# Performance work log

Measured on AMD Instinct MI355X. Metric: run time of the kernel, lower is better.

Reference implementation:

```python
import jax, jax.numpy as jnp
import numpy as np

D = 1024           # fusion_dim
H_MHA = 16         # fusion_heads
H_GAT = 8          # graph attention heads
GAT_DH = D // H_GAT
DIL = (1, 2, 4, 8, 16)
K = 7              # temporal_kernel_size
B, T = 8, 256


def setup_inputs() -> dict:
    key = jax.random.key(0)
    ks = jax.random.split(key, 20)

    def w(k, sh, fan):
        return jax.random.normal(k, sh, jnp.float32) * np.float32(1.0 / np.sqrt(fan))

    inp = {"features": jax.random.normal(ks[0], (B, T, D), jnp.float32)}
    for i, dil in enumerate(DIL):
        inp["conv_w%d" % i] = w(ks[1 + i], (D, D, K), D * K)   # torch Conv1d (out, in, k)
        inp["conv_b%d" % i] = jnp.zeros((D,), jnp.float32)
    inp["fp_w"] = w(ks[6], (D, 5 * D), 5 * D)                    # torch Linear (out, in)
    inp["fp_b"] = jnp.zeros((D,), jnp.float32)
    inp["ln_g"] = jnp.ones((D,), jnp.float32)
    inp["ln_b"] = jnp.zeros((D,), jnp.float32)
    inp["wq"] = w(ks[7], (D, D), D); inp["bq"] = jnp.zeros((D,), jnp.float32)
    inp["wk"] = w(ks[8], (D, D), D); inp["bk"] = jnp.zeros((D,), jnp.float32)
    inp["wv"] = w(ks[9], (D, D), D); inp["bv"] = jnp.zeros((D,), jnp.float32)
    inp["wo"] = w(ks[10], (D, D), D); inp["bo"] = jnp.zeros((D,), jnp.float32)
    inp["gat_w"] = w(ks[11], (D, D), D)
    inp["gat_b"] = jnp.zeros((D,), jnp.float32)
    # original `a` is (2*head_dim, 1) shared across heads; split into a1 (source) / a2 (target)
    inp["gat_a1"] = w(ks[12], (GAT_DH,), 2 * GAT_DH)
    inp["gat_a2"] = w(ks[13], (GAT_DH,), 2 * GAT_DH)
    return inp


def _forward(features, conv_ws, conv_bs, fp_w, fp_b, ln_g, ln_b,
             wq, bq, wk, bk, wv, bv, wo, bo, gat_w, gat_b, gat_a1, gat_a2):
    Bb, Tt, Dm = features.shape
    x = jnp.transpose(features, (0, 2, 1))                       # (B, D, T)
    feats = []
    for wgt, bias, dil in zip(conv_ws, conv_bs, DIL):
        pad = (K - 1) * dil // 2                                 # 'same' padding
        y = jax.lax.conv_general_dilated(
            x, wgt, window_strides=(1,), padding=[(pad, pad)],
            rhs_dilation=(dil,), dimension_numbers=("NCH", "OIH", "NCH"))
        feats.append(jnp.transpose(y + bias[None, :, None], (0, 2, 1)))
    ms = jnp.concatenate(feats, axis=-1)                         # (B, T, 5D)
    z = ms @ fp_w.T + fp_b                                       # (B, T, D)
    mu = jnp.mean(z, -1, keepdims=True)
    var = jnp.var(z, -1, keepdims=True)
    z = (z - mu) * jax.lax.rsqrt(var + 1e-5) * ln_g + ln_b       # LayerNorm
    z = jax.nn.gelu(z, approximate=False)
    # --- multi-head self attention (batch_first, no dropout at eval) ---
    dh = Dm // H_MHA
    q = (z @ wq.T + bq).reshape(Bb, Tt, H_MHA, dh)
    k = (z @ wk.T + bk).reshape(Bb, Tt, H_MHA, dh)
    v = (z @ wv.T + bv).reshape(Bb, Tt, H_MHA, dh)
    scores = jnp.einsum("bqhd,bkhd->bhqk", q, k) * np.float32(1.0 / np.sqrt(dh))
    attn = jax.nn.softmax(scores, axis=-1)
    ctx = jnp.einsum("bhqk,bkhd->bqhd", attn, v).reshape(Bb, Tt, Dm)
    att_out = ctx @ wo.T + bo
    # --- all-pairs graph attention over N = B*T nodes (GAT-style, a shared across heads) ---
    n = Bb * Tt
    hg = (att_out.reshape(n, Dm) @ gat_w.T + gat_b).reshape(n, H_GAT, GAT_DH)
    e1 = jnp.einsum("nhd,d->nh", hg, gat_a1)                     # a1 . h_i
    e2 = jnp.einsum("nhd,d->nh", hg, gat_a2)                     # a2 . h_j
    e = jax.nn.leaky_relu(e1[:, None, :] + e2[None, :, :], 0.2)  # (N, N, H) via broadcast
    alpha = jax.nn.softmax(e, axis=1)                            # normalize over j
    hp = jnp.einsum("ijh,jhd->ihd", alpha, hg).reshape(n, Dm)
    g = jax.nn.elu(hp).reshape(Bb, Tt, Dm)
    return g + features


def reference(features, conv_w0, conv_w1, conv_w2, conv_w3, conv_w4,
              conv_b0, conv_b1, conv_b2, conv_b3, conv_b4,
              fp_w, fp_b, ln_g, ln_b,
              wq, bq, wk, bk, wv, bv, wo, bo,
              gat_w, gat_b, gat_a1, gat_a2):
    return _forward(features,
                    (conv_w0, conv_w1, conv_w2, conv_w3, conv_w4),
                    (conv_b0, conv_b1, conv_b2, conv_b3, conv_b4),
                    fp_w, fp_b, ln_g, ln_b,
                    wq, bq, wk, bk, wv, bv, wo, bo,
                    gat_w, gat_b, gat_a1, gat_a2)
```

## Files before the change

kernel.cpp:

```cpp
#include <hip/hip_runtime.h>
#include <hip/hip_bf16.h>

typedef __bf16 bf16_t;
typedef bf16_t bf16x8 __attribute__((ext_vector_type(8)));
typedef bf16_t bf16x4v __attribute__((ext_vector_type(4)));
typedef float f32x4 __attribute__((ext_vector_type(4)));

__device__ __forceinline__ void gll16(const bf16_t* g, bf16_t* l) {
    __builtin_amdgcn_global_load_lds(
        (const __attribute__((address_space(1))) unsigned int*)g,
        (__attribute__((address_space(3))) unsigned int*)l, 16, 0, 0);
}

__global__ __launch_bounds__(256)
void cvt_f32_bf16(const float* __restrict__ in, bf16_t* __restrict__ out, int n4)
{
    int i = blockIdx.x * 256 + threadIdx.x;
    if (i < n4) {
        float4 v = ((const float4*)in)[i];
        bf16x4v o = { (bf16_t)v.x, (bf16_t)v.y, (bf16_t)v.z, (bf16_t)v.w };
        *(bf16x4v*)&out[i * 4] = o;
    }
}

__global__ __launch_bounds__(256)
void cvt_multi(const float* __restrict__ fpw, const float* __restrict__ wq,
               const float* __restrict__ wk, const float* __restrict__ wv,
               const float* __restrict__ wo, const float* __restrict__ gw,
               bf16_t* __restrict__ fpwb, bf16_t* __restrict__ wqb,
               bf16_t* __restrict__ wkb, bf16_t* __restrict__ wvb,
               bf16_t* __restrict__ wob, bf16_t* __restrict__ gwb)
{
    int id = blockIdx.x * 256 + threadIdx.x;
    const float* src; bf16_t* dst; int off;
    if (id < 1310720) { src = fpw; dst = fpwb; off = id; }
    else {
        int id3 = id - 1310720;
        int w = id3 >> 18; off = id3 & 262143;
        const float* ss[5] = {wq, wk, wv, wo, gw};
        bf16_t* dd[5] = {wqb, wkb, wvb, wob, gwb};
        src = ss[w]; dst = dd[w];
    }
    float4 v = ((const float4*)src)[off];
    bf16x4v o = { (bf16_t)v.x, (bf16_t)v.y, (bf16_t)v.z, (bf16_t)v.w };
    *(bf16x4v*)&dst[off * 4] = o;
}

__global__ __launch_bounds__(256)
void reorder_convw(const float* w0, const float* w1, const float* w2,
                   const float* w3, const float* w4, bf16_t* __restrict__ out)
{
    int gid = blockIdx.x * 256 + threadIdx.x;
    int i = gid / 1835008;
    int w = gid - i * 1835008;
    int o = w / 1792;
    int r2 = w - o * 1792;
    int kk = r2 >> 8, c4 = (r2 & 255) * 4;
    const float* ws[5] = {w0, w1, w2, w3, w4};
    const float* src = ws[i] + (size_t)o * 7168 + c4 * 7 + kk;
    bf16x4v v = { (bf16_t)src[0], (bf16_t)src[7], (bf16_t)src[14], (bf16_t)src[21] };
    *(bf16x4v*)&out[((size_t)(i * 7 + kk) << 20) + (o << 10) + c4] = v;
}

__global__ __launch_bounds__(256)
void gather_bias(const float* b0, const float* b1, const float* b2,
                 const float* b3, const float* b4,
                 const float* bq, const float* bk,
                 float* __restrict__ out, float* __restrict__ qkbias,
                 bf16_t* __restrict__ zp)
{
    int idx = blockIdx.x * 256 + threadIdx.x;
    if (blockIdx.x == 0 && threadIdx.x < 32) zp[threadIdx.x] = (bf16_t)0.0f;
    if (idx < 5120) {
        const float* bs[5] = {b0, b1, b2, b3, b4};
        out[idx] = bs[idx >> 10][idx & 1023];
    } else {
        int j = idx - 5120;
        qkbias[j] = (j < 1024) ? bq[j] : bk[j - 1024];
    }
}

template<bool CONV, bool OUT_BF16, bool BIAS_ROW = false, int NR = 128>
__global__ __launch_bounds__(256)
void mfma_gemm(const bf16_t* __restrict__ A, const bf16_t* __restrict__ Bw,
               const float* __restrict__ bias, void* __restrict__ outv,
               const bf16_t* __restrict__ zp,
               int Kd, int lda, int ldb, int ldo, int out_col0)
{
    constexpr int FN = NR / 32;
    __shared__ __align__(16) bf16_t As[3][NR * 32];
    __shared__ __align__(16) bf16_t Bs[3][128 * 32];
    const int t = threadIdx.x;
    const int lane = t & 63, wave = t >> 6;
    const int wn = (wave & 1) * (NR / 2), wm = (wave >> 1) * 64;
    const int q = lane >> 4, lr = lane & 15;
    const int mt = CONV ? (blockIdx.x & 7) : blockIdx.x;
    const int conv_i = CONV ? (blockIdx.x >> 3) : 0;
    const int m0 = mt * 128, n0 = blockIdx.y * NR;
    const int srow = lane >> 2, sseg = lane & 3;
    const int sw_seg = sseg ^ ((srow >> 1) & 3);
    const int slotq = (q ^ ((lr >> 1) & 3)) * 8;

    f32x4 acc[FN][4];
    #pragma unroll
    for (int a = 0; a < FN; a++)
        #pragma unroll
        for (int b = 0; b < 4; b++) acc[a][b] = (f32x4){0.f, 0.f, 0.f, 0.f};

    const int ksteps = Kd >> 5;
    const int T = CONV ? ksteps * 7 : ksteps;

    int s_tap = 0, s_k0 = 0;
    auto do_stage = [&](int bi) {
        const bf16_t* Bp = CONV ? (Bw + ((size_t)(conv_i * 7 + s_tap) << 20)) : Bw;
        const int shift = CONV ? ((s_tap - 3) << conv_i) : 0;
        #pragma unroll
        for (int p = 0; p < NR / 64; p++) {
            const int slab = p * 64 + wave * 16;
            const bf16_t* ga;
            if (CONV) {
                const int slabN = n0 + slab;
                const int inSeg = slabN & 255;
                if (inSeg + shift >= 0 && inSeg + shift <= 240) {
                    ga = A + (size_t)(slabN + srow + shift) * lda + s_k0 + sw_seg * 8;
                } else {
                    int n = slabN + srow;
                    int tg = (n & 255) + shift;
                    ga = ((unsigned)tg < 256u)
                       ? A + (size_t)((n & ~255) + tg) * lda + s_k0 + sw_seg * 8
                       : zp + sseg * 8;
                }
            } else {
                ga = A + (size_t)(n0 + slab + srow) * lda + s_k0 + sw_seg * 8;
            }
            gll16(ga, &As[bi][slab * 32]);
        }
        #pragma unroll
        for (int p = 0; p < 2; p++) {
            const int slab = p * 64 + wave * 16;
            const int rr = slab + srow;
            gll16(Bp + (size_t)(m0 + rr) * ldb + s_k0 + sw_seg * 8, &Bs[bi][slab * 32]);
        }
        s_k0 += 32;
        if (CONV && s_k0 == Kd) { s_k0 = 0; s_tap++; }
    };

    do_stage(0);
    do_stage(1);

    int cur = 0;
    for (int s = 0; s < T; s++) {
        if (s + 1 < T) {
            if constexpr (NR == 128) asm volatile("s_waitcnt vmcnt(4)" ::: "memory");
            else                     asm volatile("s_waitcnt vmcnt(3)" ::: "memory");
        } else {
            asm volatile("s_waitcnt vmcnt(0)" ::: "memory");
        }
        __builtin_amdgcn_s_barrier();
        __builtin_amdgcn_sched_barrier(0);

        bf16x8 af[FN], bfv[4];
        #pragma unroll
        for (int f = 0; f < FN; f++)
            af[f] = *(bf16x8*)&As[cur][(wn + f * 16 + lr) * 32 + slotq];
        #pragma unroll
        for (int f = 0; f < 4; f++)
            bfv[f] = *(bf16x8*)&Bs[cur][(wm + f * 16 + lr) * 32 + slotq];

        int nb = cur + 2; if (nb >= 3) nb -= 3;
        if (s + 2 < T) do_stage(nb);

        __builtin_amdgcn_s_setprio(1);
        #pragma unroll
        for (int fn = 0; fn < FN; fn++)
            #pragma unroll
            for (int fm = 0; fm < 4; fm++)
                acc[fn][fm] = __builtin_amdgcn_mfma_f32_16x16x32_bf16(
                    af[fn], bfv[fm], acc[fn][fm], 0, 0, 0);
        __builtin_amdgcn_s_setprio(0);
        cur++; if (cur == 3) cur = 0;
    }

    const int oc0 = CONV ? (conv_i << 10) : out_col0;
    #pragma unroll
    for (int fn = 0; fn < FN; fn++) {
        #pragma unroll
        for (int r = 0; r < 4; r++) {
            int n = n0 + wn + fn * 16 + q * 4 + r;
            #pragma unroll
            for (int fm = 0; fm < 4; fm++) {
                int m = m0 + wm + fm * 16 + lr;
                float v = acc[fn][fm][r];
                if (bias) v += bias[BIAS_ROW ? n : (oc0 + m)];
                if (OUT_BF16)
                    ((bf16_t*)outv)[(size_t)n * ldo + oc0 + m] = (bf16_t)v;
                else
                    ((float*)outv)[(size_t)n * ldo + oc0 + m] = v;
            }
        }
    }
}

__global__ __launch_bounds__(256)
void ln_gelu(float* __restrict__ z, bf16_t* __restrict__ zb,
             const float* __restrict__ g, const float* __restrict__ b)
{
    __shared__ float r1[256], r2[256];
    const int n = blockIdx.x, t = threadIdx.x;
    float* row = z + (size_t)n * 1024;
    float x[4], s = 0.f, s2 = 0.f;
    #pragma unroll
    for (int u = 0; u < 4; u++) {
        x[u] = row[t + u * 256];
        s += x[u]; s2 += x[u] * x[u];
    }
    r1[t] = s; r2[t] = s2;
    __syncthreads();
    for (int off = 128; off > 0; off >>= 1) {
        if (t < off) { r1[t] += r1[t + off]; r2[t] += r2[t + off]; }
        __syncthreads();
    }
    const float mu  = r1[0] * (1.0f / 1024.0f);
    const float var = r2[0] * (1.0f / 1024.0f) - mu * mu;
    const float rstd = rsqrtf(var + 1e-5f);
    #pragma unroll
    for (int u = 0; u < 4; u++) {
        int c = t + u * 256;
        float y = (x[u] - mu) * rstd * g[c] + b[c];
        float gv = 0.5f * y * (1.0f + erff(y * 0.70710678118654752f));
        row[c] = gv;
        zb[(size_t)n * 1024 + c] = (bf16_t)gv;
    }
}

__global__ __launch_bounds__(256)
void attn_mfma(const bf16_t* __restrict__ qg, const bf16_t* __restrict__ kg,
               const bf16_t* __restrict__ vt, bf16_t* __restrict__ ctx)
{
    const int it = blockIdx.x, h = blockIdx.y, bb = blockIdx.z;
    const int t = threadIdx.x, lane = t & 63, wave = t >> 6;
    const int q4 = lane >> 4, lr = lane & 15;
    const size_t qkbase = (size_t)bb * 256 * 2048 + (size_t)h * 64;

    __shared__ __align__(16) bf16_t Qs[4][32 * 64];
    __shared__ __align__(16) bf16_t Ks[64 * 64];
    __shared__ __align__(16) bf16_t Vs[64 * 64];
    __shared__ __align__(16) bf16_t Ps[4][32 * 64];

    {
        const int itbase = it * 128;
        #pragma unroll
        for (int rep = 0; rep < 4; rep++) {
            int idx = rep * 256 + t;
            int rl = idx >> 3, seg = idx & 7;
            bf16x8 v = *(const bf16x8*)&qg[qkbase + (size_t)(itbase + rl) * 2048 + seg * 8];
            *(bf16x8*)&Qs[rl >> 5][(rl & 31) * 64 + ((seg ^ (rl & 7)) << 3)] = v;
        }
    }

    f32x4 o[2][4];
    float mrow[2][4], lrow[2][4];
    #pragma unroll
    for (int fn = 0; fn < 2; fn++)
        #pragma unroll
        for (int x = 0; x < 4; x++) {
            o[fn][x] = (f32x4){0.f, 0.f, 0.f, 0.f};
            mrow[fn][x] = -1e30f; lrow[fn][x] = 0.f;
        }

    for (int j0 = 0; j0 < 256; j0 += 64) {
        __syncthreads();
        #pragma unroll
        for (int rep = 0; rep < 2; rep++) {
            int idx = rep * 256 + t;
            int rl = idx >> 3, seg = idx & 7;
            bf16x8 kv = *(const bf16x8*)&kg[qkbase + (size_t)(j0 + rl) * 2048 + seg * 8];
            *(bf16x8*)&Ks[rl * 64 + ((seg ^ (rl & 7)) << 3)] = kv;
            bf16x8 vv = *(const bf16x8*)&vt[(size_t)(h * 64 + rl) * 2048 + bb * 256 + j0 + seg * 8];
            *(bf16x8*)&Vs[rl * 64 + ((seg ^ (rl & 7)) << 3)] = vv;
        }
        __syncthreads();

        f32x4 s[2][4];
        #pragma unroll
        for (int fn = 0; fn < 2; fn++)
            #pragma unroll
            for (int fm = 0; fm < 4; fm++) s[fn][fm] = (f32x4){0.f, 0.f, 0.f, 0.f};
        #pragma unroll
        for (int kk = 0; kk < 2; kk++) {
            bf16x8 aq[2], bk[4];
            #pragma unroll
            for (int fn = 0; fn < 2; fn++) {
                int row = fn * 16 + lr;
                aq[fn] = *(bf16x8*)&Qs[wave][row * 64 + (((kk * 4 + q4) ^ (row & 7)) << 3)];
            }
            #pragma unroll
            for (int fm = 0; fm < 4; fm++) {
                int row = fm * 16 + lr;
                bk[fm] = *(bf16x8*)&Ks[row * 64 + (((kk * 4 + q4) ^ (row & 7)) << 3)];
            }
            #pragma unroll
            for (int fn = 0; fn < 2; fn++)
                #pragma unroll
                for (int fm = 0; fm < 4; fm++)
                    s[fn][fm] = __builtin_amdgcn_mfma_f32_16x16x32_bf16(
                        aq[fn], bk[fm], s[fn][fm], 0, 0, 0);
        }

        #pragma unroll
        for (int fn = 0; fn < 2; fn++) {
            #pragma unroll
            for (int r = 0; r < 4; r++) {
                float sv[4];
                #pragma unroll
                for (int fm = 0; fm < 4; fm++) sv[fm] = s[fn][fm][r] * 0.125f;
                float rm = fmaxf(fmaxf(sv[0], sv[1]), fmaxf(sv[2], sv[3]));
                rm = fmaxf(rm, __shfl_xor(rm, 1));
                rm = fmaxf(rm, __shfl_xor(rm, 2));
                rm = fmaxf(rm, __shfl_xor(rm, 4));
                rm = fmaxf(rm, __shfl_xor(rm, 8));
                float mold = mrow[fn][r];
                float mnew = fmaxf(mold, rm);
                float scl = __expf(mold - mnew);
                mrow[fn][r] = mnew;
                int prow = fn * 16 + q4 * 4 + r;
                float psum = 0.f;
                #pragma unroll
                for (int fm = 0; fm < 4; fm++) {
                    float p = __expf(sv[fm] - mnew);
                    psum += p;
                    int col = fm * 16 + lr;
                    Ps[wave][prow * 64 + (col ^ ((prow & 7) << 3))] = (bf16_t)p;
                }
                psum += __shfl_xor(psum, 1);
                psum += __shfl_xor(psum, 2);
                psum += __shfl_xor(psum, 4);
                psum += __shfl_xor(psum, 8);
                lrow[fn][r] = lrow[fn][r] * scl + psum;
                #pragma unroll
                for (int fd = 0; fd < 4; fd++) o[fn][fd][r] *= scl;
            }
        }

        #pragma unroll
        for (int kk = 0; kk < 2; kk++) {
            bf16x8 ap[2], bvf[4];
            #pragma unroll
            for (int fn = 0; fn < 2; fn++) {
                int row = fn * 16 + lr;
                ap[fn] = *(bf16x8*)&Ps[wave][row * 64 + (((kk * 4 + q4) ^ (row & 7)) << 3)];
            }
            #pragma unroll
            for (int fd = 0; fd < 4; fd++) {
                int row = fd * 16 + lr;
                bvf[fd] = *(bf16x8*)&Vs[row * 64 + (((kk * 4 + q4) ^ (row & 7)) << 3)];
            }
            #pragma unroll
            for (int fn = 0; fn < 2; fn++)
                #pragma unroll
                for (int fd = 0; fd < 4; fd++)
                    o[fn][fd] = __builtin_amdgcn_mfma_f32_16x16x32_bf16(
                        ap[fn], bvf[fd], o[fn][fd], 0, 0, 0);
        }
    }

    const int i0 = it * 128 + wave * 32;
    #pragma unroll
    for (int fn = 0; fn < 2; fn++) {
        #pragma unroll
        for (int r = 0; r < 4; r++) {
            float inv = 1.0f / lrow[fn][r];
            int row = i0 + fn * 16 + q4 * 4 + r;
            #pragma unroll
            for (int fd = 0; fd < 4; fd++) {
                int col = h * 64 + fd * 16 + lr;
                ctx[(size_t)bb * 262144 + (size_t)row * 1024 + col] =
                    (bf16_t)(o[fn][fd][r] * inv);
            }
        }
    }
}

__global__ __launch_bounds__(256)
void gat_e(const float* __restrict__ hg, const float* __restrict__ a1,
           const float* __restrict__ a2, float* __restrict__ e1t,
           float* __restrict__ e2t)
{
    int id = blockIdx.x * 256 + threadIdx.x;
    int h = id >> 11, n = id & 2047;
    const float* hr = hg + (size_t)n * 1024 + h * 128;
    float s1 = 0.f, s2 = 0.f;
    for (int d = 0; d < 128; d += 4) {
        float4 x = *(const float4*)&hr[d];
        float4 u1 = *(const float4*)&a1[d];
        float4 u2 = *(const float4*)&a2[d];
        s1 += x.x * u1.x + x.y * u1.y + x.z * u1.z + x.w * u1.w;
        s2 += x.x * u2.x + x.y * u2.y + x.z * u2.z + x.w * u2.w;
    }
    e1t[id] = s1; e2t[id] = s2;
}

__global__ __launch_bounds__(256)
void transpose_hg(const float* __restrict__ in, bf16_t* __restrict__ out)
{
    __shared__ float tile[32][33];
    const int t = threadIdx.x;
    const int j0 = blockIdx.x * 32, c0 = blockIdx.y * 32;
    {
        int jl = t >> 3, cl = (t & 7) * 4;
        float4 v = *(const float4*)(in + (size_t)(j0 + jl) * 1024 + c0 + cl);
        tile[jl][cl] = v.x; tile[jl][cl + 1] = v.y;
        tile[jl][cl + 2] = v.z; tile[jl][cl + 3] = v.w;
    }
    __syncthreads();
    {
        int cl = t >> 3, jl = (t & 7) * 4;
        bf16x4v o = { (bf16_t)tile[jl][cl], (bf16_t)tile[jl + 1][cl],
                      (bf16_t)tile[jl + 2][cl], (bf16_t)tile[jl + 3][cl] };
        *(bf16x4v*)&out[(size_t)(c0 + cl) * 2048 + j0 + jl] = o;
    }
}

__global__ __launch_bounds__(256)
void gat_agg_mfma(const bf16_t* __restrict__ hgT, const float* __restrict__ e1t,
                  const float* __restrict__ e2t, const float* __restrict__ feat,
                  float* __restrict__ outp)
{
    const int it = blockIdx.x, h = blockIdx.y;
    const int i0 = it * 64;
    __shared__ float e2s[2048];
    __shared__ float e1s[64], mS[64], lSinv[64];
    __shared__ float wmax[4];
    __shared__ __align__(16) bf16_t Ps[64 * 136];
    __shared__ __align__(16) bf16_t Hs[128 * 136];
    const int t = threadIdx.x;
    const int lane = t & 63, wave = t >> 6;
    const int q = lane >> 4, lr = lane & 15;
    const int wm = wave * 32;

    float lmax = -1e30f;
    for (int idx = t; idx < 2048; idx += 256) {
        float v = e2t[h * 2048 + idx];
        e2s[idx] = v;
        lmax = fmaxf(lmax, v);
    }
    if (t < 64) e1s[t] = e1t[h * 2048 + i0 + t];
    #pragma unroll
    for (int d = 1; d < 64; d <<= 1) lmax = fmaxf(lmax, __shfl_xor(lmax, d));
    if (lane == 0) wmax[wave] = lmax;
    __syncthreads();
    {
        float maxE2 = fmaxf(fmaxf(wmax[0], wmax[1]), fmaxf(wmax[2], wmax[3]));
        if (t < 64) {
            float x = e1s[t] + maxE2;
            mS[t] = (x >= 0.f) ? x : 0.2f * x;
        }
    }
    __syncthreads();

    f32x4 acc[4][2];
    #pragma unroll
    for (int a = 0; a < 4; a++)
        #pragma unroll
        for (int b = 0; b < 2; b++) acc[a][b] = (f32x4){0.f, 0.f, 0.f, 0.f};
    float psum[4] = {0.f, 0.f, 0.f, 0.f};

    for (int j0 = 0; j0 < 2048; j0 += 128) {
        for (int idx = t; idx < 2048; idx += 256) {
            int d = idx >> 4, seg = idx & 15;
            *(bf16x8*)&Hs[d * 136 + seg * 8] =
                *(const bf16x8*)&hgT[(size_t)(h * 128 + d) * 2048 + j0 + seg * 8];
        }
        #pragma unroll
        for (int rep = 0; rep < 4; rep++) {
            int idx = rep * 256 + t;
            int i = idx >> 4, jg = idx & 15;
            float ei = e1s[i], mi = mS[i];
            bf16x8 pv;
            #pragma unroll
            for (int u = 0; u < 8; u++) {
                float x = ei + e2s[j0 + jg * 8 + u];
                x = (x >= 0.f) ? x : 0.2f * x;
                float p = __expf(x - mi);
                psum[rep] += p;
                pv[u] = (bf16_t)p;
            }
            *(bf16x8*)&Ps[i * 136 + jg * 8] = pv;
        }
        __syncthreads();
        #pragma unroll
        for (int kb = 0; kb < 4; kb++) {
            bf16x8 af[4], bf2[2];
            #pragma unroll
            for (int fn = 0; fn < 4; fn++)
                af[fn] = *(bf16x8*)&Ps[(fn * 16 + lr) * 136 + kb * 32 + q * 8];
            #pragma unroll
            for (int fm = 0; fm < 2; fm++)
                bf2[fm] = *(bf16x8*)&Hs[(wm + fm * 16 + lr) * 136 + kb * 32 + q * 8];
            #pragma unroll
            for (int fn = 0; fn < 4; fn++)
                #pragma unroll
                for (int fm = 0; fm < 2; fm++)
                    acc[fn][fm] = __builtin_amdgcn_mfma_f32_16x16x32_bf16(
                        af[fn], bf2[fm], acc[fn][fm], 0, 0, 0);
        }
        __syncthreads();
    }

    #pragma unroll
    for (int rep = 0; rep < 4; rep++) {
        float v = psum[rep];
        v += __shfl_xor(v, 1);
        v += __shfl_xor(v, 2);
        v += __shfl_xor(v, 4);
        v += __shfl_xor(v, 8);
        if ((t & 15) == 0) lSinv[rep * 16 + (t >> 4)] = 1.0f / v;
    }
    __syncthreads();

    #pragma unroll
    for (int fn = 0; fn < 4; fn++) {
        #pragma unroll
        for (int r = 0; r < 4; r++) {
            int il = fn * 16 + q * 4 + r;
            int i = i0 + il;
            float inv = lSinv[il];
            #pragma unroll
            for (int fm = 0; fm < 2; fm++) {
                int col = h * 128 + wm + fm * 16 + lr;
                float v = acc[fn][fm][r] * inv;
                v = (v > 0.f) ? v : (expf(v) - 1.0f);
                size_t off = (size_t)i * 1024 + col;
                outp[off] = v + feat[off];
            }
        }
    }
}

extern "C" void kernel_launch(void* const* d_in, const int* in_sizes, int n_in,
                              void* d_out, int out_size, void* d_ws, size_t ws_size,
                              hipStream_t stream)
{
    const float* feat = (const float*)d_in[0];
    const float *cw[5], *cb[5];
    if (in_sizes[2] == 1024) {
        for (int i = 0; i < 5; i++) { cw[i] = (const float*)d_in[1 + 2*i]; cb[i] = (const float*)d_in[2 + 2*i]; }
    } else {
        for (int i = 0; i < 5; i++) { cw[i] = (const float*)d_in[1 + i];   cb[i] = (const float*)d_in[6 + i]; }
    }
    const float* fp_w = (const float*)d_in[11];
    const float* fp_b = (const float*)d_in[12];
    const float* ln_g = (const float*)d_in[13];
    const float* ln_b = (const float*)d_in[14];
    const float* wq = (const float*)d_in[15]; const float* bq = (const float*)d_in[16];
    const float* wk = (const float*)d_in[17]; const float* bk = (const float*)d_in[18];
    const float* wv = (const float*)d_in[19]; const float* bv = (const float*)d_in[20];
    const float* wo = (const float*)d_in[21]; const float* bo = (const float*)d_in[22];
    const float* gat_w = (const float*)d_in[23]; const float* gat_b = (const float*)d_in[24];
    const float* ga1 = (const float*)d_in[25]; const float* ga2 = (const float*)d_in[26];
    float* outp = (float*)d_out;

    char* wsb = (char*)d_ws;
    bf16_t* xb    = (bf16_t*)(wsb);
    bf16_t* msb   = (bf16_t*)(wsb + 4194304);
    bf16_t* wcb   = (bf16_t*)(wsb + 25165824);
    float*  zf    = (float*) (wsb + 98566144);
    bf16_t* zb    = (bf16_t*)(wsb + 106954752);
    bf16_t* qb    = (bf16_t*)(wsb + 111149056);
    bf16_t* kb    = (bf16_t*)(wsb + 115343360);
    bf16_t* vb    = (bf16_t*)(wsb + 119537664);
    float*  cball = (float*) (wsb + 123731968);
    float*  e1t   = (float*) (wsb + 123752448);
    float*  e2t   = (float*) (wsb + 123817984);
    bf16_t* zpage = (bf16_t*)(wsb + 123883520);
    bf16_t* fpwb = wcb;
    bf16_t* wqb  = wcb + 5242880;
    bf16_t* wkb  = wqb + 1048576;
    bf16_t* wvb  = wkb + 1048576;
    bf16_t* wob  = wvb + 1048576;
    bf16_t* gwb  = wob + 1048576;
    bf16_t* qkb  = qb;
    float*  qkbias = e1t;
    bf16_t* ctxb = zb;
    bf16_t* attb = kb;
    float*  hgb  = zf;
    bf16_t* hgtb = msb;

    const dim3 blk(256);

    cvt_f32_bf16<<<dim3(2048), blk, 0, stream>>>(feat, xb, 524288);
    reorder_convw<<<dim3(35840), blk, 0, stream>>>(cw[0], cw[1], cw[2], cw[3], cw[4], wcb);
    gather_bias<<<dim3(28), blk, 0, stream>>>(cb[0], cb[1], cb[2], cb[3], cb[4],
                                              bq, bk, cball, qkbias, zpage);

    mfma_gemm<true, true><<<dim3(40, 16), blk, 0, stream>>>(
        xb, wcb, cball, msb, zpage, 1024, 1024, 1024, 5120, 0);

    cvt_multi<<<dim3(10240), blk, 0, stream>>>(fp_w, wq, wk, wv, wo, gat_w,
                                               fpwb, wqb, wkb, wvb, wob, gwb);

    mfma_gemm<false, false, false, 64><<<dim3(8, 32), blk, 0, stream>>>(
        msb, fpwb, fp_b, zf, zpage, 5120, 5120, 5120, 1024, 0);

    ln_gelu<<<dim3(2048), blk, 0, stream>>>(zf, zb, ln_g, ln_b);

    mfma_gemm<false, true><<<dim3(16, 16), blk, 0, stream>>>(
        zb, wqb, qkbias, qkb, zpage, 1024, 1024, 1024, 2048, 0);
    mfma_gemm<false, true, true, 64><<<dim3(16, 16), blk, 0, stream>>>(
        wvb, zb, bv, vb, zpage, 1024, 1024, 1024, 2048, 0);

    attn_mfma<<<dim3(2, 16, 8), blk, 0, stream>>>(qkb, qkb + 1024, vb, ctxb);

    mfma_gemm<false, true, false, 64><<<dim3(8, 32), blk, 0, stream>>>(
        ctxb, wob, bo, attb, zpage, 1024, 1024, 1024, 1024, 0);

    mfma_gemm<false, false, false, 64><<<dim3(8, 32), blk, 0, stream>>>(
        attb, gwb, gat_b, hgb, zpage, 1024, 1024, 1024, 1024, 0);

    transpose_hg<<<dim3(64, 32), blk, 0, stream>>>(hgb, hgtb);
    gat_e<<<dim3(64), blk, 0, stream>>>(hgb, ga1, ga2, e1t, e2t);
    gat_agg_mfma<<<dim3(32, 8), blk, 0, stream>>>(hgtb, e1t, e2t, feat, outp);
}
```

Measured before the change: 752.1 us.

## Fold output projection into GAT weight and emit transposed hg directly

```diff
diff --git a/kernel.cpp b/kernel.cpp
--- a/kernel.cpp
+++ b/kernel.cpp
@@ -26,10 +26,10 @@
 __global__ __launch_bounds__(256)
 void cvt_multi(const float* __restrict__ fpw, const float* __restrict__ wq,
                const float* __restrict__ wk, const float* __restrict__ wv,
-               const float* __restrict__ wo, const float* __restrict__ gw,
+               const float* __restrict__ gw,
                bf16_t* __restrict__ fpwb, bf16_t* __restrict__ wqb,
                bf16_t* __restrict__ wkb, bf16_t* __restrict__ wvb,
-               bf16_t* __restrict__ wob, bf16_t* __restrict__ gwb)
+               bf16_t* __restrict__ gwb)
 {
     int id = blockIdx.x * 256 + threadIdx.x;
     const float* src; bf16_t* dst; int off;
@@ -37,8 +37,8 @@
     else {
         int id3 = id - 1310720;
         int w = id3 >> 18; off = id3 & 262143;
-        const float* ss[5] = {wq, wk, wv, wo, gw};
-        bf16_t* dd[5] = {wqb, wkb, wvb, wob, gwb};
+        const float* ss[4] = {wq, wk, wv, gw};
+        bf16_t* dd[4] = {wqb, wkb, wvb, gwb};
         src = ss[w]; dst = dd[w];
     }
     float4 v = ((const float4*)src)[off];
@@ -51,15 +51,13 @@
                    const float* w3, const float* w4, bf16_t* __restrict__ out)
 {
     int gid = blockIdx.x * 256 + threadIdx.x;
-    int i = gid / 1835008;
-    int w = gid - i * 1835008;
-    int o = w / 1792;
-    int r2 = w - o * 1792;
-    int kk = r2 >> 8, c4 = (r2 & 255) * 4;
+    int i = gid >> 20, rem = gid & 1048575;
+    int o = rem >> 10, c = rem & 1023;
     const float* ws[5] = {w0, w1, w2, w3, w4};
-    const float* src = ws[i] + (size_t)o * 7168 + c4 * 7 + kk;
-    bf16x4v v = { (bf16_t)src[0], (bf16_t)src[7], (bf16_t)src[14], (bf16_t)src[21] };
-    *(bf16x4v*)&out[((size_t)(i * 7 + kk) << 20) + (o << 10) + c4] = v;
+    const float* src = ws[i] + (size_t)o * 7168 + c * 7;
+    #pragma unroll
+    for (int kk = 0; kk < 7; kk++)
+        out[((size_t)(i * 7 + kk) << 20) + (o << 10) + c] = (bf16_t)src[kk];
 }
 
 __global__ __launch_bounds__(256)
@@ -78,6 +76,46 @@
         int j = idx - 5120;
         qkbias[j] = (j < 1024) ? bq[j] : bk[j - 1024];
     }
+}
+
+__global__ __launch_bounds__(256)
+void transpose_w(const float* __restrict__ in, bf16_t* __restrict__ out)
+{
+    __shared__ float tile[32][33];
+    const int t = threadIdx.x;
+    const int j0 = blockIdx.x * 32, c0 = blockIdx.y * 32;
+    {
+        int jl = t >> 3, cl = (t & 7) * 4;
+        float4 v = *(const float4*)(in + (size_t)(j0 + jl) * 1024 + c0 + cl);
+        tile[jl][cl] = v.x; tile[jl][cl + 1] = v.y;
+        tile[jl][cl + 2] = v.z; tile[jl][cl + 3] = v.w;
+    }
+    __syncthreads();
+    {
+        int cl = t >> 3, jl = (t & 7) * 4;
+        bf16x4v o = { (bf16_t)tile[jl][cl], (bf16_t)tile[jl + 1][cl],
+                      (bf16_t)tile[jl + 2][cl], (bf16_t)tile[jl + 3][cl] };
+        *(bf16x4v*)&out[(size_t)(c0 + cl) * 1024 + j0 + jl] = o;
+    }
+}
+
+__global__ __launch_bounds__(256)
+void fold_bias(const float* __restrict__ gw, const float* __restrict__ bo,
+               const float* __restrict__ gb, float* __restrict__ bc)
+{
+    const int wave = threadIdx.x >> 6, lane = threadIdx.x & 63;
+    const int d = blockIdx.x * 4 + wave;
+    const float* row = gw + (size_t)d * 1024;
+    float s = 0.f;
+    #pragma unroll
+    for (int k = lane * 4; k < 1024; k += 256) {
+        float4 x = *(const float4*)&row[k];
+        float4 a = *(const float4*)&bo[k];
+        s += x.x * a.x + x.y * a.y + x.z * a.z + x.w * a.w;
+    }
+    s += __shfl_xor(s, 1);  s += __shfl_xor(s, 2);  s += __shfl_xor(s, 4);
+    s += __shfl_xor(s, 8);  s += __shfl_xor(s, 16); s += __shfl_xor(s, 32);
+    if (lane == 0) bc[d] = gb[d] + s;
 }
 
 template<bool CONV, bool OUT_BF16, bool BIAS_ROW = false, int NR = 128>
@@ -382,43 +420,21 @@
 }
 
 __global__ __launch_bounds__(256)
-void gat_e(const float* __restrict__ hg, const float* __restrict__ a1,
+void gat_e(const bf16_t* __restrict__ hgT, const float* __restrict__ a1,
            const float* __restrict__ a2, float* __restrict__ e1t,
            float* __restrict__ e2t)
 {
     int id = blockIdx.x * 256 + threadIdx.x;
     int h = id >> 11, n = id & 2047;
-    const float* hr = hg + (size_t)n * 1024 + h * 128;
+    const bf16_t* base = hgT + (size_t)(h * 128) * 2048 + n;
     float s1 = 0.f, s2 = 0.f;
-    for (int d = 0; d < 128; d += 4) {
-        float4 x = *(const float4*)&hr[d];
-        float4 u1 = *(const float4*)&a1[d];
-        float4 u2 = *(const float4*)&a2[d];
-        s1 += x.x * u1.x + x.y * u1.y + x.z * u1.z + x.w * u1.w;
-        s2 += x.x * u2.x + x.y * u2.y + x.z * u2.z + x.w * u2.w;
+    #pragma unroll 4
+    for (int d = 0; d < 128; d++) {
+        float x = (float)base[(size_t)d * 2048];
+        s1 += x * a1[d];
+        s2 += x * a2[d];
     }
     e1t[id] = s1; e2t[id] = s2;
-}
-
-__global__ __launch_bounds__(256)
-void transpose_hg(const float* __restrict__ in, bf16_t* __restrict__ out)
-{
-    __shared__ float tile[32][33];
-    const int t = threadIdx.x;
-    const int j0 = blockIdx.x * 32, c0 = blockIdx.y * 32;
-    {
-        int jl = t >> 3, cl = (t & 7) * 4;
-        float4 v = *(const float4*)(in + (size_t)(j0 + jl) * 1024 + c0 + cl);
-        tile[jl][cl] = v.x; tile[jl][cl + 1] = v.y;
-        tile[jl][cl + 2] = v.z; tile[jl][cl + 3] = v.w;
-    }
-    __syncthreads();
-    {
-        int cl = t >> 3, jl = (t & 7) * 4;
-        bf16x4v o = { (bf16_t)tile[jl][cl], (bf16_t)tile[jl + 1][cl],
-                      (bf16_t)tile[jl + 2][cl], (bf16_t)tile[jl + 3][cl] };
-        *(bf16x4v*)&out[(size_t)(c0 + cl) * 2048 + j0 + jl] = o;
-    }
 }
 
 __global__ __launch_bounds__(256)
@@ -577,47 +593,48 @@
     bf16_t* wqb  = wcb + 5242880;
     bf16_t* wkb  = wqb + 1048576;
     bf16_t* wvb  = wkb + 1048576;
-    bf16_t* wob  = wvb + 1048576;
-    bf16_t* gwb  = wob + 1048576;
+    bf16_t* woTb = wvb + 1048576;
+    bf16_t* gwb  = woTb + 1048576;
     bf16_t* qkb  = qb;
     float*  qkbias = e1t;
     bf16_t* ctxb = zb;
-    bf16_t* attb = kb;
-    float*  hgb  = zf;
+    bf16_t* wcomb = xb;
+    float*  bcomb = cball;
     bf16_t* hgtb = msb;
 
     const dim3 blk(256);
 
     cvt_f32_bf16<<<dim3(2048), blk, 0, stream>>>(feat, xb, 524288);
-    reorder_convw<<<dim3(35840), blk, 0, stream>>>(cw[0], cw[1], cw[2], cw[3], cw[4], wcb);
+    reorder_convw<<<dim3(20480), blk, 0, stream>>>(cw[0], cw[1], cw[2], cw[3], cw[4], wcb);
     gather_bias<<<dim3(28), blk, 0, stream>>>(cb[0], cb[1], cb[2], cb[3], cb[4],
                                               bq, bk, cball, qkbias, zpage);
 
     mfma_gemm<true, true><<<dim3(40, 16), blk, 0, stream>>>(
         xb, wcb, cball, msb, zpage, 1024, 1024, 1024, 5120, 0);
 
-    cvt_multi<<<dim3(10240), blk, 0, stream>>>(fp_w, wq, wk, wv, wo, gat_w,
-                                               fpwb, wqb, wkb, wvb, wob, gwb);
+    cvt_multi<<<dim3(9216), blk, 0, stream>>>(fp_w, wq, wk, wv, gat_w,
+                                              fpwb, wqb, wkb, wvb, gwb);
+    transpose_w<<<dim3(32, 32), blk, 0, stream>>>(wo, woTb);
+    fold_bias<<<dim3(256), blk, 0, stream>>>(gat_w, bo, gat_b, bcomb);
+
+    mfma_gemm<false, true, false, 64><<<dim3(8, 16), blk, 0, stream>>>(
+        gwb, woTb, nullptr, wcomb, zpage, 1024, 1024, 1024, 1024, 0);
 
     mfma_gemm<false, false, false, 64><<<dim3(8, 32), blk, 0, stream>>>(
         msb, fpwb, fp_b, zf, zpage, 5120, 5120, 5120, 1024, 0);
 
     ln_gelu<<<dim3(2048), blk, 0, stream>>>(zf, zb, ln_g, ln_b);
 
-    mfma_gemm<false, true><<<dim3(16, 16), blk, 0, stream>>>(
+    mfma_gemm<false, true, false, 64><<<dim3(16, 32), blk, 0, stream>>>(
         zb, wqb, qkbias, qkb, zpage, 1024, 1024, 1024, 2048, 0);
     mfma_gemm<false, true, true, 64><<<dim3(16, 16), blk, 0, stream>>>(
         wvb, zb, bv, vb, zpage, 1024, 1024, 1024, 2048, 0);
 
     attn_mfma<<<dim3(2, 16, 8), blk, 0, stream>>>(qkb, qkb + 1024, vb, ctxb);
 
-    mfma_gemm<false, true, false, 64><<<dim3(8, 32), blk, 0, stream>>>(
-        ctxb, wob, bo, attb, zpage, 1024, 1024, 1024, 1024, 0);
-
-    mfma_gemm<false, false, false, 64><<<dim3(8, 32), blk, 0, stream>>>(
-        attb, gwb, gat_b, hgb, zpage, 1024, 1024, 1024, 1024, 0);
-
-    transpose_hg<<<dim3(64, 32), blk, 0, stream>>>(hgb, hgtb);
-    gat_e<<<dim3(64), blk, 0, stream>>>(hgb, ga1, ga2, e1t, e2t);
+    mfma_gemm<false, true, true, 64><<<dim3(16, 16), blk, 0, stream>>>(
+        wcomb, ctxb, bcomb, hgtb, zpage, 1024, 1024, 1024, 2048, 0);
+
+    gat_e<<<dim3(64), blk, 0, stream>>>(hgtb, ga1, ga2, e1t, e2t);
     gat_agg_mfma<<<dim3(32, 8), blk, 0, stream>>>(hgtb, e1t, e2t, feat, outp);
 }
```

Result: faster. 658.6 us (-12.4%).
